# Optimization experiments

Measured on AMD Instinct MI355X. Metric: run time of the kernel, lower is better.

Reference implementation:

```python
import jax, jax.numpy as jnp
import numpy as np

N = 100000  # nodes
E = 3200000  # edges
NEG_SLOPE = 0.2  # GATConv default


def _gat_conv(x, src, dst, edge_attr, W, a_src, a_dst, W_e, a_e, bias):
    """PyG GATConv, heads=1, concat=True, add_self_loops=True (fill_value='mean')."""
    n = x.shape[0]
    loop = jnp.arange(n)
    s = jnp.concatenate([src, loop])
    d = jnp.concatenate([dst, loop])
    mean_ea = edge_attr.mean(axis=0)
    ea = jnp.concatenate([edge_attr, jnp.broadcast_to(mean_ea, (n, edge_attr.shape[1]))], axis=0)
    h = x @ W                          # [N, C]
    al_src = h @ a_src                 # [N]
    al_dst = h @ a_dst                 # [N]
    he = ea @ W_e                      # [E+N, C]
    alpha = al_src[s] + al_dst[d] + he @ a_e   # [E+N]
    alpha = jax.nn.leaky_relu(alpha, NEG_SLOPE)
    amax = jax.ops.segment_max(alpha, d, num_segments=n)
    ex = jnp.exp(alpha - amax[d])
    denom = jax.ops.segment_sum(ex, d, num_segments=n)
    coef = ex / (denom[d] + 1e-16)     # per-destination softmax (PyG softmax)
    out = jax.ops.segment_sum(h[s] * coef[:, None], d, num_segments=n)
    return out + bias


def _edge_mlp(z, w0, b0, w1, b1, w2, b2, w3, b3):
    z = jax.nn.relu(z @ w0 + b0)
    z = jax.nn.relu(z @ w1 + b1)
    z = jax.nn.relu(z @ w2 + b2)
    return z @ w3 + b3


def setup_inputs() -> dict:
    key = jax.random.key(0)
    ks = jax.random.split(key, 24)
    g = lambda i, sh, s=0.1: jax.random.normal(ks[i], sh, dtype=jnp.float32) * s
    return {
        "x": g(0, (N, 4), 1.0),
        "edge_attr": g(1, (E, 3), 1.0),
        "W1": g(2, (4, 16), 0.5), "as1": g(3, (16,)), "ad1": g(4, (16,)),
        "We1": g(5, (3, 16), 0.5), "ae1": g(6, (16,)), "b1": g(7, (16,)),
        "mw0": g(8, (35, 16), 0.17), "mb0": g(9, (16,)),
        "mw1": g(10, (16, 16), 0.25), "mb1": g(11, (16,)),
        "mw2": g(12, (16, 8), 0.25), "mb2": g(13, (8,)),
        "mw3": g(14, (8, 4), 0.35), "mb3": g(15, (4,)),
        "W2": g(16, (16, 2), 0.25), "as2": g(17, (2,)), "ad2": g(18, (2,)),
        "We2": g(19, (4, 2), 0.5), "ae2": g(20, (2,)), "b2": g(21, (2,)),
        "edge_index": jax.random.randint(ks[22], (2, E), 0, N),
    }


def reference(x, edge_attr, W1, as1, ad1, We1, ae1, b1,
              mw0, mb0, mw1, mb1, mw2, mb2, mw3, mb3,
              W2, as2, ad2, We2, ae2, b2, edge_index):
    src, dst = edge_index[0], edge_index[1]
    h = _gat_conv(x, src, dst, edge_attr, W1, as1, ad1, We1, ae1, b1)      # [N, 16]
    z = jnp.concatenate([h[src], edge_attr, h[dst]], axis=1)               # [E, 35]
    e = _edge_mlp(z, mw0, mb0, mw1, mb1, mw2, mb2, mw3, mb3)               # [E, 4]
    out = _gat_conv(h, src, dst, e, W2, as2, ad2, We2, ae2, b2)            # [N, 2]
    return jax.nn.log_softmax(out, axis=1), jax.nn.log_softmax(e, axis=1)
```

## Files before the change

### kernel.cpp

```cpp
#include <hip/hip_runtime.h>
#include <hip/hip_bf16.h>
#include <stdint.h>

typedef __hip_bfloat16 bf16;
typedef unsigned long long ull;
#define NT 256
#define EPT 4

__device__ __forceinline__ float b2f(bf16 v){ return __bfloat162float(v); }
__device__ __forceinline__ bf16 f2b(float v){ return __float2bfloat16(v); }
__device__ __forceinline__ float lrelu(float a){ return a>0.f ? a : 0.2f*a; }
__device__ __forceinline__ float sanf(float v){ return __builtin_isfinite(v) ? v : -12345.f; }
__device__ __forceinline__ float us2f(unsigned short u){ return __uint_as_float(((unsigned)u)<<16); }
__device__ __forceinline__ unsigned short f2bu(float v){ bf16 b=f2b(v); unsigned short u; __builtin_memcpy(&u,&b,2); return u; }

__device__ __forceinline__ float ld(const void* p, size_t i, int f32in){
  return f32in ? ((const float*)p)[i] : b2f(((const bf16*)p)[i]);
}

__device__ __forceinline__ float waveReduceSum(float v){
#pragma unroll
  for(int o=32;o>0;o>>=1) v += __shfl_down(v,o,64);
  return v;
}

__device__ __forceinline__ unsigned clampi(int v, int n){
  unsigned u=(unsigned)v; return (u<(unsigned)n)?u:0u;
}

__device__ __forceinline__ void load_h1v(const bf16* h1, unsigned node, float* dst){
  const ull* p=(const ull*)(h1+(size_t)node*16);
#pragma unroll
  for(int q=0;q<4;q++){
    ull v=p[q];
    dst[q*4+0]=us2f((unsigned short)v);        dst[q*4+1]=us2f((unsigned short)(v>>16));
    dst[q*4+2]=us2f((unsigned short)(v>>32));  dst[q*4+3]=us2f((unsigned short)(v>>48));
  }
}
__device__ __forceinline__ void load_x4(const void* x, unsigned n, int f32in, float* o){
  if(f32in){ float4 v=((const float4*)x)[n]; o[0]=v.x;o[1]=v.y;o[2]=v.z;o[3]=v.w; }
  else{
    ull v=((const ull*)x)[n];
    o[0]=us2f((unsigned short)v);       o[1]=us2f((unsigned short)(v>>16));
    o[2]=us2f((unsigned short)(v>>32)); o[3]=us2f((unsigned short)(v>>48));
  }
}

__global__ __launch_bounds__(64) void k_probe(const unsigned short* __restrict__ xraw,
                                              int nscan, float* __restrict__ stats){
  int t=threadIdx.x;
  int bad=0;
  for(int k=t*8;k<t*8+8;k++){
    if(k<nscan){
      unsigned short u=xraw[k];
      unsigned ex=(u>>7)&0xFF;
      bool plaus = (ex==0u) || (ex>=97u && ex<=157u);
      if(!plaus) bad++;
    }
  }
#pragma unroll
  for(int o=32;o>0;o>>=1) bad += __shfl_down(bad,o,64);
  if(t==0){
    for(int i=0;i<7;i++) stats[i]=0.f;
    ((int*)stats)[7] = (bad>=8) ? 1 : 0;
  }
}

__global__ __launch_bounds__(NT) void k_prep(const void* __restrict__ ea,
                                             const int* __restrict__ idx,
                                             int* __restrict__ rowc,
                                             float* __restrict__ stats, int E, int N){
  const int f32in=((const int*)stats)[7];
  __shared__ float lds[16];
  float s0=0.f,s1=0.f,s2=0.f;
  for(size_t e=(size_t)blockIdx.x*NT+threadIdx.x; e<(size_t)E; e+=(size_t)gridDim.x*NT){
    s0+=ld(ea,e*3+0,f32in); s1+=ld(ea,e*3+1,f32in); s2+=ld(ea,e*3+2,f32in);
    unsigned d=clampi(idx[(size_t)E+e],N);
    atomicAdd(&rowc[d],1);
  }
  int lane=threadIdx.x&63, wv=threadIdx.x>>6;
  s0=waveReduceSum(s0); s1=waveReduceSum(s1); s2=waveReduceSum(s2);
  if(lane==0){ lds[wv*4+0]=s0; lds[wv*4+1]=s1; lds[wv*4+2]=s2; }
  __syncthreads();
  if(threadIdx.x==0){
    float a0=0,a1=0,a2=0;
    for(int w=0;w<NT/64;w++){ a0+=lds[w*4]; a1+=lds[w*4+1]; a2+=lds[w*4+2]; }
    atomicAdd(&stats[0],a0); atomicAdd(&stats[1],a1); atomicAdd(&stats[2],a2);
  }
}

__global__ __launch_bounds__(NT) void k_node1(
    const void* __restrict__ x, const void* __restrict__ W1,
    const void* __restrict__ as1, const void* __restrict__ ad1,
    const float* __restrict__ stats,
    float* __restrict__ als, float* __restrict__ ald, int N){
  const int f32in=((const int*)stats)[7];
  __shared__ float sW1[64], sas[16], sad[16];
  if(threadIdx.x<64) sW1[threadIdx.x]=ld(W1,threadIdx.x,f32in);
  if(threadIdx.x<16){ sas[threadIdx.x]=ld(as1,threadIdx.x,f32in); sad[threadIdx.x]=ld(ad1,threadIdx.x,f32in); }
  __syncthreads();
  int i=blockIdx.x*NT+threadIdx.x;
  if(i>=N) return;
  float xv[4]; load_x4(x,(unsigned)i,f32in,xv);
  float a_s=0.f,a_d=0.f;
#pragma unroll
  for(int j=0;j<16;j++){
    float v=xv[0]*sW1[j]+xv[1]*sW1[16+j]+xv[2]*sW1[32+j]+xv[3]*sW1[48+j];
    a_s+=v*sas[j]; a_d+=v*sad[j];
  }
  als[i]=a_s; ald[i]=a_d;
}

__global__ __launch_bounds__(NT) void k_scan1(const int* __restrict__ rowc, int* __restrict__ bsum, int N){
  __shared__ int sm[NT];
  int i=blockIdx.x*NT+threadIdx.x;
  sm[threadIdx.x]=(i<N)?rowc[i]:0;
  __syncthreads();
  for(int o=NT/2;o>0;o>>=1){ if(threadIdx.x<o) sm[threadIdx.x]+=sm[threadIdx.x+o]; __syncthreads(); }
  if(threadIdx.x==0) bsum[blockIdx.x]=sm[0];
}
__global__ __launch_bounds__(1024) void k_scan2(int* __restrict__ bsum, int NB){
  __shared__ int sm[1024];
  int i=threadIdx.x;
  int v=(i<NB)?bsum[i]:0;
  sm[i]=v; __syncthreads();
  for(int o=1;o<1024;o<<=1){
    int t=(i>=o)?sm[i-o]:0; __syncthreads();
    sm[i]+=t; __syncthreads();
  }
  if(i<NB) bsum[i]=(i==0)?0:sm[i-1];
}
__global__ __launch_bounds__(NT) void k_scan3(int* __restrict__ rowc, const int* __restrict__ bsum, int N){
  __shared__ int sm[NT];
  int i=blockIdx.x*NT+threadIdx.x;
  int v=(i<N)?rowc[i]:0;
  sm[threadIdx.x]=v; __syncthreads();
  for(int o=1;o<NT;o<<=1){
    int t=(threadIdx.x>=o)?sm[threadIdx.x-o]:0; __syncthreads();
    sm[threadIdx.x]+=t; __syncthreads();
  }
  if(i<N) rowc[i]=bsum[blockIdx.x]+sm[threadIdx.x]-v;
}

__global__ __launch_bounds__(NT) void k_scatter(
    const int* __restrict__ idx, const void* __restrict__ ea,
    const void* __restrict__ We1, const void* __restrict__ ae1,
    const float* __restrict__ als, const float* __restrict__ stats,
    int* __restrict__ rowc, ull* __restrict__ csr, int E, int N){
  const int f32in=((const int*)stats)[7];
  __shared__ float sve[3];
  if(threadIdx.x<3){
    float v=0.f;
    for(int j=0;j<16;j++) v+=ld(We1,threadIdx.x*16+j,f32in)*ld(ae1,j,f32in);
    sve[threadIdx.x]=v;
  }
  __syncthreads();
  int e=blockIdx.x*NT+threadIdx.x;
  if(e>=E) return;
  unsigned s=clampi(idx[e],N), d=clampi(idx[(size_t)E+e],N);
  float ap = als[s] + ld(ea,(size_t)e*3+0,f32in)*sve[0]
                    + ld(ea,(size_t)e*3+1,f32in)*sve[1]
                    + ld(ea,(size_t)e*3+2,f32in)*sve[2];
  int pos=atomicAdd(&rowc[d],1);
  csr[pos] = (ull)s | ((ull)__float_as_uint(ap)<<32);
}

__global__ __launch_bounds__(NT) void k_gather1(
    const ull* __restrict__ csr, const int* __restrict__ rowe,
    const float* __restrict__ als, const float* __restrict__ ald,
    const void* __restrict__ x, const void* __restrict__ W1, const void* __restrict__ b1,
    const void* __restrict__ W2, const void* __restrict__ as2, const void* __restrict__ ad2,
    const void* __restrict__ We1, const void* __restrict__ ae1,
    const float* __restrict__ stats, float invE,
    bf16* __restrict__ h1, float* __restrict__ h2,
    float* __restrict__ als2, float* __restrict__ ald2, int N){
  const int f32in=((const int*)stats)[7];
  __shared__ float sW1[64], sb1[16], sW2[32], sas2[2], sad2[2], saea[1];
  if(threadIdx.x<64) sW1[threadIdx.x]=ld(W1,threadIdx.x,f32in);
  if(threadIdx.x<16) sb1[threadIdx.x]=ld(b1,threadIdx.x,f32in);
  if(threadIdx.x<32) sW2[threadIdx.x]=ld(W2,threadIdx.x,f32in);
  if(threadIdx.x<2){ sas2[threadIdx.x]=ld(as2,threadIdx.x,f32in); sad2[threadIdx.x]=ld(ad2,threadIdx.x,f32in); }
  if(threadIdx.x==0){
    float a=0.f;
    for(int k=0;k<3;k++){
      float v=0.f;
      for(int j=0;j<16;j++) v+=ld(We1,k*16+j,f32in)*ld(ae1,j,f32in);
      a+=stats[k]*v;
    }
    saea[0]=a*invE;
  }
  __syncthreads();
  int n=blockIdx.x*16+(threadIdx.x>>4);
  int c=threadIdx.x&15;
  if(n>=N) return;
  int end=rowe[n];
  int start=(n==0)?0:rowe[n-1];
  float aldn=ald[n], alsn=als[n];
  float aself=lrelu(alsn+aldn+saea[0]);
  float w0=sW1[c], w1=sW1[16+c], w2=sW1[32+c], w3=sW1[48+c];
  float m=aself;
  for(int k=start+c;k<end;k+=16){
    float ap=__uint_as_float((unsigned)(csr[k]>>32));
    m=fmaxf(m,lrelu(ap+aldn));
  }
#pragma unroll
  for(int o=1;o<16;o<<=1) m=fmaxf(m,__shfl_xor(m,o,64));
  float xv[4]; load_x4(x,(unsigned)n,f32in,xv);
  float hc_self=xv[0]*w0+xv[1]*w1+xv[2]*w2+xv[3]*w3;
  float exs=expf(fminf(aself-m,0.f));
  float den=exs, acc=exs*hc_self;
  for(int k=start;k<end;k++){
    ull v=csr[k];
    unsigned src=(unsigned)(v&0xffffffffu);
    float ap=__uint_as_float((unsigned)(v>>32));
    float ex=expf(fminf(lrelu(ap+aldn)-m,0.f));
    den+=ex;
    float xs[4]; load_x4(x,src,f32in,xs);
    float hc=xs[0]*w0+xs[1]*w1+xs[2]*w2+xs[3]*w3;
    acc+=ex*hc;
  }
  float inv=1.f/(den+1e-16f);
  float h1c=acc*inv+sb1[c];
  h1[(size_t)n*16+c]=f2b(h1c);
  float r0=h1c*sW2[c*2+0], r1=h1c*sW2[c*2+1];
#pragma unroll
  for(int o=1;o<16;o<<=1){ r0+=__shfl_xor(r0,o,64); r1+=__shfl_xor(r1,o,64); }
  if(c==0){
    h2[(size_t)n*2+0]=r0; h2[(size_t)n*2+1]=r1;
    als2[n]=r0*sas2[0]+r1*sas2[1];
    ald2[n]=r0*sad2[0]+r1*sad2[1];
  }
}

__global__ __launch_bounds__(NT) void k_wprep(
    const void* mw0,const void* mb0,const void* mw1,const void* mb1,
    const void* mw2,const void* mb2,const void* mw3,const void* mb3,
    const void* We2,const void* ae2,
    const float* __restrict__ stats, float* __restrict__ gw){
  const int f32in=((const int*)stats)[7];
  for(int t=threadIdx.x;t<560;t+=NT) gw[t]=ld(mw0,t,f32in);
  for(int t=threadIdx.x;t<256;t+=NT) gw[576+t]=ld(mw1,t,f32in);
  for(int t=threadIdx.x;t<128;t+=NT) gw[848+t]=ld(mw2,t,f32in);
  if(threadIdx.x<32) gw[984+threadIdx.x]=ld(mw3,threadIdx.x,f32in);
  if(threadIdx.x<16){ gw[560+threadIdx.x]=ld(mb0,threadIdx.x,f32in); gw[832+threadIdx.x]=ld(mb1,threadIdx.x,f32in); }
  if(threadIdx.x<8) gw[976+threadIdx.x]=ld(mb2,threadIdx.x,f32in);
  if(threadIdx.x<4){
    gw[1016+threadIdx.x]=ld(mb3,threadIdx.x,f32in);
    gw[1020+threadIdx.x]=ld(We2,threadIdx.x*2+0,f32in)*ld(ae2,0,f32in)
                        +ld(We2,threadIdx.x*2+1,f32in)*ld(ae2,1,f32in);
  }
}

__device__ __forceinline__ void mlp_eval_g4(const float z[EPT][35],
                                            const float* __restrict__ gw,
                                            float ev[EPT][4]){
  const float4* w4=(const float4*)gw;
  float t1[EPT][16];
  {
    const float4* b=(const float4*)(gw+560);
    float4 b0=b[0],b1=b[1],b2=b[2],b3=b[3];
#pragma unroll
    for(int u=0;u<EPT;u++){
      t1[u][0]=b0.x; t1[u][1]=b0.y; t1[u][2]=b0.z; t1[u][3]=b0.w;
      t1[u][4]=b1.x; t1[u][5]=b1.y; t1[u][6]=b1.z; t1[u][7]=b1.w;
      t1[u][8]=b2.x; t1[u][9]=b2.y; t1[u][10]=b2.z; t1[u][11]=b2.w;
      t1[u][12]=b3.x; t1[u][13]=b3.y; t1[u][14]=b3.z; t1[u][15]=b3.w;
    }
  }
#pragma unroll
  for(int i2=0;i2<35;i2++){
    float4 r0=w4[i2*4+0], r1=w4[i2*4+1], r2=w4[i2*4+2], r3=w4[i2*4+3];
#pragma unroll
    for(int u=0;u<EPT;u++){
      float a=z[u][i2];
      t1[u][0]+=a*r0.x; t1[u][1]+=a*r0.y; t1[u][2]+=a*r0.z; t1[u][3]+=a*r0.w;
      t1[u][4]+=a*r1.x; t1[u][5]+=a*r1.y; t1[u][6]+=a*r1.z; t1[u][7]+=a*r1.w;
      t1[u][8]+=a*r2.x; t1[u][9]+=a*r2.y; t1[u][10]+=a*r2.z; t1[u][11]+=a*r2.w;
      t1[u][12]+=a*r3.x; t1[u][13]+=a*r3.y; t1[u][14]+=a*r3.z; t1[u][15]+=a*r3.w;
    }
  }
#pragma unroll
  for(int u=0;u<EPT;u++)
#pragma unroll
    for(int j=0;j<16;j++) t1[u][j]=fmaxf(t1[u][j],0.f);

  const float4* w14=(const float4*)(gw+576);
  float t2[EPT][16];
  {
    const float4* b=(const float4*)(gw+832);
    float4 b0=b[0],b1=b[1],b2=b[2],b3=b[3];
#pragma unroll
    for(int u=0;u<EPT;u++){
      t2[u][0]=b0.x; t2[u][1]=b0.y; t2[u][2]=b0.z; t2[u][3]=b0.w;
      t2[u][4]=b1.x; t2[u][5]=b1.y; t2[u][6]=b1.z; t2[u][7]=b1.w;
      t2[u][8]=b2.x; t2[u][9]=b2.y; t2[u][10]=b2.z; t2[u][11]=b2.w;
      t2[u][12]=b3.x; t2[u][13]=b3.y; t2[u][14]=b3.z; t2[u][15]=b3.w;
    }
  }
#pragma unroll
  for(int i2=0;i2<16;i2++){
    float4 r0=w14[i2*4+0], r1=w14[i2*4+1], r2=w14[i2*4+2], r3=w14[i2*4+3];
#pragma unroll
    for(int u=0;u<EPT;u++){
      float a=t1[u][i2];
      t2[u][0]+=a*r0.x; t2[u][1]+=a*r0.y; t2[u][2]+=a*r0.z; t2[u][3]+=a*r0.w;
      t2[u][4]+=a*r1.x; t2[u][5]+=a*r1.y; t2[u][6]+=a*r1.z; t2[u][7]+=a*r1.w;
      t2[u][8]+=a*r2.x; t2[u][9]+=a*r2.y; t2[u][10]+=a*r2.z; t2[u][11]+=a*r2.w;
      t2[u][12]+=a*r3.x; t2[u][13]+=a*r3.y; t2[u][14]+=a*r3.z; t2[u][15]+=a*r3.w;
    }
  }
#pragma unroll
  for(int u=0;u<EPT;u++)
#pragma unroll
    for(int j=0;j<16;j++) t2[u][j]=fmaxf(t2[u][j],0.f);

  const float4* w24=(const float4*)(gw+848);
  float t3[EPT][8];
  {
    const float4* b=(const float4*)(gw+976);
    float4 b0=b[0],b1=b[1];
#pragma unroll
    for(int u=0;u<EPT;u++){
      t3[u][0]=b0.x; t3[u][1]=b0.y; t3[u][2]=b0.z; t3[u][3]=b0.w;
      t3[u][4]=b1.x; t3[u][5]=b1.y; t3[u][6]=b1.z; t3[u][7]=b1.w;
    }
  }
#pragma unroll
  for(int i2=0;i2<16;i2++){
    float4 r0=w24[i2*2+0], r1=w24[i2*2+1];
#pragma unroll
    for(int u=0;u<EPT;u++){
      float a=t2[u][i2];
      t3[u][0]+=a*r0.x; t3[u][1]+=a*r0.y; t3[u][2]+=a*r0.z; t3[u][3]+=a*r0.w;
      t3[u][4]+=a*r1.x; t3[u][5]+=a*r1.y; t3[u][6]+=a*r1.z; t3[u][7]+=a*r1.w;
    }
  }
#pragma unroll
  for(int u=0;u<EPT;u++)
#pragma unroll
    for(int j=0;j<8;j++) t3[u][j]=fmaxf(t3[u][j],0.f);

  const float4* w34=(const float4*)(gw+984);
  {
    const float4* b=(const float4*)(gw+1016);
    float4 b0=b[0];
#pragma unroll
    for(int u=0;u<EPT;u++){ ev[u][0]=b0.x; ev[u][1]=b0.y; ev[u][2]=b0.z; ev[u][3]=b0.w; }
  }
#pragma unroll
  for(int i2=0;i2<8;i2++){
    float4 r0=w34[i2];
#pragma unroll
    for(int u=0;u<EPT;u++){
      float a=t3[u][i2];
      ev[u][0]+=a*r0.x; ev[u][1]+=a*r0.y; ev[u][2]+=a*r0.z; ev[u][3]+=a*r0.w;
    }
  }
}

__device__ __forceinline__ void edge_epi(const float* ev, unsigned s, unsigned d, int e,
                                         const float* __restrict__ gw,
                                         const float* __restrict__ als2,
                                         const float* __restrict__ ald2,
                                         const float* __restrict__ h2,
                                         float* __restrict__ denom2, float* __restrict__ acc2,
                                         void* __restrict__ d_out, int f32in, int N){
  float m=fmaxf(fmaxf(ev[0],ev[1]),fmaxf(ev[2],ev[3]));
  float lse=m+logf(expf(ev[0]-m)+expf(ev[1]-m)+expf(ev[2]-m)+expf(ev[3]-m));
  if(f32in){
    float4 o; o.x=sanf(ev[0]-lse); o.y=sanf(ev[1]-lse); o.z=sanf(ev[2]-lse); o.w=sanf(ev[3]-lse);
    ((float4*)((float*)d_out+(size_t)2*N))[e]=o;
  }else{
    ull o = (ull)f2bu(sanf(ev[0]-lse))
          | ((ull)f2bu(sanf(ev[1]-lse))<<16)
          | ((ull)f2bu(sanf(ev[2]-lse))<<32)
          | ((ull)f2bu(sanf(ev[3]-lse))<<48);
    ((ull*)((bf16*)d_out+(size_t)2*N))[e]=o;
  }
  const float* s_ve2=gw+1020;
  float adot=ev[0]*s_ve2[0]+ev[1]*s_ve2[1]+ev[2]*s_ve2[2]+ev[3]*s_ve2[3];
  float a2=sanf(lrelu(als2[s]+ald2[d]+adot));
  float ex=expf(fminf(a2,80.f));
  float2 h2s=((const float2*)h2)[s];
  atomicAdd(&denom2[d],ex);
  atomicAdd(&acc2[(size_t)d*2+0],ex*h2s.x);
  atomicAdd(&acc2[(size_t)d*2+1],ex*h2s.y);
}

__global__ __launch_bounds__(NT,1) void k_edge2(
    const int* __restrict__ idx, const void* __restrict__ ea,
    const bf16* __restrict__ h1,
    const float* __restrict__ als2, const float* __restrict__ ald2,
    const float* __restrict__ gw,
    const float* __restrict__ h2,
    float* __restrict__ denom2, float* __restrict__ acc2,
    float* __restrict__ stats, void* __restrict__ d_out, int E, int N){
  const int f32in=((const int*)stats)[7];
  __shared__ float s_red[16];
  size_t base=(size_t)blockIdx.x*(NT*EPT)+threadIdx.x;
  int e[EPT]; bool v[EPT]; int es[EPT]; unsigned s[EPT], d[EPT];
#pragma unroll
  for(int u=0;u<EPT;u++){
    e[u]=(int)(base+(size_t)u*NT);
    v[u]=e[u]<E;
    es[u]=v[u]?e[u]:0;
    s[u]=clampi(idx[es[u]],N);
    d[u]=clampi(idx[(size_t)E+es[u]],N);
  }
  float z[EPT][35];
#pragma unroll
  for(int u=0;u<EPT;u++){
    load_h1v(h1,s[u],z[u]);
    load_h1v(h1,d[u],z[u]+19);
    z[u][16]=ld(ea,(size_t)es[u]*3+0,f32in);
    z[u][17]=ld(ea,(size_t)es[u]*3+1,f32in);
    z[u][18]=ld(ea,(size_t)es[u]*3+2,f32in);
  }
  float ev[EPT][4];
  mlp_eval_g4(z,gw,ev);
  float c0=0.f,c1=0.f,c2=0.f,c3=0.f;
#pragma unroll
  for(int u=0;u<EPT;u++){
    if(v[u]){
      edge_epi(ev[u],s[u],d[u],e[u],gw,als2,ald2,h2,denom2,acc2,d_out,f32in,N);
      c0+=ev[u][0]; c1+=ev[u][1]; c2+=ev[u][2]; c3+=ev[u][3];
    }
  }
  int lane=threadIdx.x&63, wv=threadIdx.x>>6;
  c0=waveReduceSum(c0); c1=waveReduceSum(c1); c2=waveReduceSum(c2); c3=waveReduceSum(c3);
  __syncthreads();
  if(lane==0){ s_red[wv*4]=c0; s_red[wv*4+1]=c1; s_red[wv*4+2]=c2; s_red[wv*4+3]=c3; }
  __syncthreads();
  if(threadIdx.x==0){
    float a0=0,a1=0,a2=0,a3=0;
    for(int w=0;w<NT/64;w++){ a0+=s_red[w*4]; a1+=s_red[w*4+1]; a2+=s_red[w*4+2]; a3+=s_red[w*4+3]; }
    atomicAdd(&stats[3],a0); atomicAdd(&stats[4],a1); atomicAdd(&stats[5],a2); atomicAdd(&stats[6],a3);
  }
}

__global__ __launch_bounds__(NT) void k_final(
    const float* __restrict__ stats, float invE,
    const float* __restrict__ als2, const float* __restrict__ ald2,
    const void* __restrict__ We2, const void* __restrict__ ae2,
    const float* __restrict__ h2,
    const float* __restrict__ denom2, const float* __restrict__ acc2,
    const void* __restrict__ bias2, void* __restrict__ d_out, int N){
  const int f32in=((const int*)stats)[7];
  __shared__ float s_ve2[4], s_b2[2];
  if(threadIdx.x<4)
    s_ve2[threadIdx.x]=ld(We2,threadIdx.x*2+0,f32in)*ld(ae2,0,f32in)
                      +ld(We2,threadIdx.x*2+1,f32in)*ld(ae2,1,f32in);
  if(threadIdx.x<2) s_b2[threadIdx.x]=ld(bias2,threadIdx.x,f32in);
  __syncthreads();
  int i=blockIdx.x*NT+threadIdx.x;
  if(i>=N) return;
  float adot=(stats[3]*s_ve2[0]+stats[4]*s_ve2[1]+stats[5]*s_ve2[2]+stats[6]*s_ve2[3])*invE;
  float self=lrelu(als2[i]+ald2[i]+adot);
  float ex=expf(fminf(self,80.f));
  float den=denom2[i]+ex;
  float inv=1.f/(den+1e-16f);
  float o0=(acc2[(size_t)i*2+0]+ex*h2[(size_t)i*2+0])*inv+s_b2[0];
  float o1=(acc2[(size_t)i*2+1]+ex*h2[(size_t)i*2+1])*inv+s_b2[1];
  float m=fmaxf(o0,o1);
  float lse=m+logf(expf(o0-m)+expf(o1-m));
  float r0=sanf(o0-lse), r1=sanf(o1-lse);
  if(f32in){
    float* o=(float*)d_out;
    o[(size_t)i*2+0]=r0; o[(size_t)i*2+1]=r1;
  }else{
    bf16* o=(bf16*)d_out;
    o[(size_t)i*2+0]=f2b(r0); o[(size_t)i*2+1]=f2b(r1);
  }
}

extern "C" void kernel_launch(void* const* d_in, const int* in_sizes, int n_in,
                              void* d_out, int out_size, void* d_ws, size_t ws_size,
                              hipStream_t stream){
  const void* x   =d_in[0];
  const void* ea  =d_in[1];
  const void* W1  =d_in[2];
  const void* as1 =d_in[3];
  const void* ad1 =d_in[4];
  const void* We1 =d_in[5];
  const void* ae1 =d_in[6];
  const void* b1  =d_in[7];
  const void* mw0 =d_in[8];
  const void* mb0 =d_in[9];
  const void* mw1 =d_in[10];
  const void* mb1 =d_in[11];
  const void* mw2 =d_in[12];
  const void* mb2 =d_in[13];
  const void* mw3 =d_in[14];
  const void* mb3 =d_in[15];
  const void* W2  =d_in[16];
  const void* as2 =d_in[17];
  const void* ad2 =d_in[18];
  const void* We2 =d_in[19];
  const void* ae2 =d_in[20];
  const void* bias2=d_in[21];
  const int*  idx =(const int*)d_in[22];

  int N=in_sizes[0]/4;
  int E=in_sizes[1]/3;
  float invE=1.f/(float)E;

  float*    F     =(float*)d_ws;
  float*    stats =F;
  float*    als   =F+8;
  float*    ald   =als+N;
  float*    ald2  =ald+N;
  int*      rowc  =(int*)(ald2+N);
  bf16*     h1    =(bf16*)(rowc+N);
  float*    h2    =(float*)(h1+(size_t)16*N);
  float*    acc2  =h2+(size_t)2*N;
  float*    den2  =ald;
  float*    gw    =(float*)((((uintptr_t)rowc)+15)&~(uintptr_t)15);

  ull* csr =(ull*)((char*)d_out+(size_t)4*N);
  int* bsum=(int*)((char*)d_out+(size_t)4*N);

  int NBn=(N+NT-1)/NT, nbE=(E+NT-1)/NT;
  int nbE4=(E+NT*EPT-1)/(NT*EPT);
  int nscan=in_sizes[0]*2; if(nscan>512) nscan=512;

  hipMemsetAsync(rowc,0,(size_t)N*sizeof(int),stream);
  k_probe  <<<1,64,0,stream>>>((const unsigned short*)x,nscan,stats);
  k_prep   <<<1024,NT,0,stream>>>(ea,idx,rowc,stats,E,N);
  k_node1  <<<NBn,NT,0,stream>>>(x,W1,as1,ad1,stats,als,ald,N);
  k_scan1  <<<NBn,NT,0,stream>>>(rowc,bsum,N);
  k_scan2  <<<1,1024,0,stream>>>(bsum,NBn);
  k_scan3  <<<NBn,NT,0,stream>>>(rowc,bsum,N);
  k_scatter<<<nbE,NT,0,stream>>>(idx,ea,We1,ae1,als,stats,rowc,csr,E,N);
  k_gather1<<<(N+15)/16,NT,0,stream>>>(csr,rowc,als,ald,x,W1,b1,W2,as2,ad2,We1,ae1,
                                       stats,invE,h1,h2,als,ald2,N);
  k_wprep  <<<1,NT,0,stream>>>(mw0,mb0,mw1,mb1,mw2,mb2,mw3,mb3,We2,ae2,stats,gw);
  hipMemsetAsync(den2,0,(size_t)N*sizeof(float),stream);
  hipMemsetAsync(acc2,0,(size_t)2*N*sizeof(float),stream);
  k_edge2  <<<nbE4,NT,0,stream>>>(idx,ea,h1,als,ald2,gw,h2,den2,acc2,stats,d_out,E,N);
  k_final  <<<NBn,NT,0,stream>>>(stats,invE,als,ald2,We2,ae2,h2,den2,acc2,bias2,d_out,N);
}
```

Before: 1.159 ms.

## Precompute per-node first MLP layer projections to cut per-edge FLOPs

Splits the first edge-MLP layer algebraically: the h[src] and h[dst] parts of the 35x16 product are computed once per node in a new kernel (k_upre) and stored as fp32 16-wide vectors. The edge kernel then gathers these two vectors, adds the 3-feature edge_attr term and the bias, and runs the remaining layers. This replaces 32 of the 35 input rows of per-edge multiply-adds with node-level work. In exchange each edge gathers 128 bytes of fp32 instead of 64 bytes of bf16 h1, and the edge kernel now uses launch_bounds(NT,2). The old path is kept as a fallback when the workspace is too small.

After: 1.134 ms. -2.2%, faster.

```diff
diff --git a/kernel.cpp b/kernel.cpp
--- a/kernel.cpp
+++ b/kernel.cpp
@@ -251,11 +251,127 @@
   }
 }
 
-__device__ __forceinline__ void mlp_eval_g4(const float z[EPT][35],
-                                            const float* __restrict__ gw,
-                                            float ev[EPT][4]){
+__global__ __launch_bounds__(NT) void k_upre(
+    const bf16* __restrict__ h1, const float* __restrict__ gw,
+    float* __restrict__ us, float* __restrict__ ud, int N){
+  int n=blockIdx.x*NT+threadIdx.x;
+  if(n>=N) return;
+  float h[16]; load_h1v(h1,(unsigned)n,h);
   const float4* w4=(const float4*)gw;
-  float t1[EPT][16];
+  float4 a0,a1,a2,a3;
+  { const float4* b=(const float4*)(gw+560); a0=b[0]; a1=b[1]; a2=b[2]; a3=b[3]; }
+#pragma unroll
+  for(int i=0;i<16;i++){
+    float z=h[i];
+    float4 r0=w4[i*4+0],r1=w4[i*4+1],r2=w4[i*4+2],r3=w4[i*4+3];
+    a0.x+=z*r0.x; a0.y+=z*r0.y; a0.z+=z*r0.z; a0.w+=z*r0.w;
+    a1.x+=z*r1.x; a1.y+=z*r1.y; a1.z+=z*r1.z; a1.w+=z*r1.w;
+    a2.x+=z*r2.x; a2.y+=z*r2.y; a2.z+=z*r2.z; a2.w+=z*r2.w;
+    a3.x+=z*r3.x; a3.y+=z*r3.y; a3.z+=z*r3.z; a3.w+=z*r3.w;
+  }
+  float4* po=(float4*)(us+(size_t)n*16);
+  po[0]=a0; po[1]=a1; po[2]=a2; po[3]=a3;
+  float4 c0=make_float4(0,0,0,0), c1=c0, c2=c0, c3=c0;
+#pragma unroll
+  for(int i=0;i<16;i++){
+    float z=h[i];
+    int r=19+i;
+    float4 r0=w4[r*4+0],r1=w4[r*4+1],r2=w4[r*4+2],r3=w4[r*4+3];
+    c0.x+=z*r0.x; c0.y+=z*r0.y; c0.z+=z*r0.z; c0.w+=z*r0.w;
+    c1.x+=z*r1.x; c1.y+=z*r1.y; c1.z+=z*r1.z; c1.w+=z*r1.w;
+    c2.x+=z*r2.x; c2.y+=z*r2.y; c2.z+=z*r2.z; c2.w+=z*r2.w;
+    c3.x+=z*r3.x; c3.y+=z*r3.y; c3.z+=z*r3.z; c3.w+=z*r3.w;
+  }
+  float4* pd=(float4*)(ud+(size_t)n*16);
+  pd[0]=c0; pd[1]=c1; pd[2]=c2; pd[3]=c3;
+}
+
+__device__ __forceinline__ void mlp_tail4(float t1[EPT][16],
+                                          const float* __restrict__ gw,
+                                          float ev[EPT][4]){
+#pragma unroll
+  for(int u=0;u<EPT;u++)
+#pragma unroll
+    for(int j=0;j<16;j++) t1[u][j]=fmaxf(t1[u][j],0.f);
+
+  const float4* w14=(const float4*)(gw+576);
+  float t2[EPT][16];
+  {
+    const float4* b=(const float4*)(gw+832);
+    float4 b0=b[0],b1=b[1],b2=b[2],b3=b[3];
+#pragma unroll
+    for(int u=0;u<EPT;u++){
+      t2[u][0]=b0.x; t2[u][1]=b0.y; t2[u][2]=b0.z; t2[u][3]=b0.w;
+      t2[u][4]=b1.x; t2[u][5]=b1.y; t2[u][6]=b1.z; t2[u][7]=b1.w;
+      t2[u][8]=b2.x; t2[u][9]=b2.y; t2[u][10]=b2.z; t2[u][11]=b2.w;
+      t2[u][12]=b3.x; t2[u][13]=b3.y; t2[u][14]=b3.z; t2[u][15]=b3.w;
+    }
+  }
+#pragma unroll
+  for(int i2=0;i2<16;i2++){
+    float4 r0=w14[i2*4+0], r1=w14[i2*4+1], r2=w14[i2*4+2], r3=w14[i2*4+3];
+#pragma unroll
+    for(int u=0;u<EPT;u++){
+      float a=t1[u][i2];
+      t2[u][0]+=a*r0.x; t2[u][1]+=a*r0.y; t2[u][2]+=a*r0.z; t2[u][3]+=a*r0.w;
+      t2[u][4]+=a*r1.x; t2[u][5]+=a*r1.y; t2[u][6]+=a*r1.z; t2[u][7]+=a*r1.w;
+      t2[u][8]+=a*r2.x; t2[u][9]+=a*r2.y; t2[u][10]+=a*r2.z; t2[u][11]+=a*r2.w;
+      t2[u][12]+=a*r3.x; t2[u][13]+=a*r3.y; t2[u][14]+=a*r3.z; t2[u][15]+=a*r3.w;
+    }
+  }
+#pragma unroll
+  for(int u=0;u<EPT;u++)
+#pragma unroll
+    for(int j=0;j<16;j++) t2[u][j]=fmaxf(t2[u][j],0.f);
+
+  const float4* w24=(const float4*)(gw+848);
+  float t3[EPT][8];
+  {
+    const float4* b=(const float4*)(gw+976);
+    float4 b0=b[0],b1=b[1];
+#pragma unroll
+    for(int u=0;u<EPT;u++){
+      t3[u][0]=b0.x; t3[u][1]=b0.y; t3[u][2]=b0.z; t3[u][3]=b0.w;
+      t3[u][4]=b1.x; t3[u][5]=b1.y; t3[u][6]=b1.z; t3[u][7]=b1.w;
+    }
+  }
+#pragma unroll
+  for(int i2=0;i2<16;i2++){
+    float4 r0=w24[i2*2+0], r1=w24[i2*2+1];
+#pragma unroll
+    for(int u=0;u<EPT;u++){
+      float a=t2[u][i2];
+      t3[u][0]+=a*r0.x; t3[u][1]+=a*r0.y; t3[u][2]+=a*r0.z; t3[u][3]+=a*r0.w;
+      t3[u][4]+=a*r1.x; t3[u][5]+=a*r1.y; t3[u][6]+=a*r1.z; t3[u][7]+=a*r1.w;
+    }
+  }
+#pragma unroll
+  for(int u=0;u<EPT;u++)
+#pragma unroll
+    for(int j=0;j<8;j++) t3[u][j]=fmaxf(t3[u][j],0.f);
+
+  const float4* w34=(const float4*)(gw+984);
+  {
+    const float4* b=(const float4*)(gw+1016);
+    float4 b0=b[0];
+#pragma unroll
+    for(int u=0;u<EPT;u++){ ev[u][0]=b0.x; ev[u][1]=b0.y; ev[u][2]=b0.z; ev[u][3]=b0.w; }
+  }
+#pragma unroll
+  for(int i2=0;i2<8;i2++){
+    float4 r0=w34[i2];
+#pragma unroll
+    for(int u=0;u<EPT;u++){
+      float a=t3[u][i2];
+      ev[u][0]+=a*r0.x; ev[u][1]+=a*r0.y; ev[u][2]+=a*r0.z; ev[u][3]+=a*r0.w;
+    }
+  }
+}
+
+__device__ __forceinline__ void mlp_head_full4(const float z[EPT][35],
+                                               const float* __restrict__ gw,
+                                               float t1[EPT][16]){
+  const float4* w4=(const float4*)gw;
   {
     const float4* b=(const float4*)(gw+560);
     float4 b0=b[0],b1=b[1],b2=b[2],b3=b[3];
@@ -277,83 +393,6 @@
       t1[u][4]+=a*r1.x; t1[u][5]+=a*r1.y; t1[u][6]+=a*r1.z; t1[u][7]+=a*r1.w;
       t1[u][8]+=a*r2.x; t1[u][9]+=a*r2.y; t1[u][10]+=a*r2.z; t1[u][11]+=a*r2.w;
       t1[u][12]+=a*r3.x; t1[u][13]+=a*r3.y; t1[u][14]+=a*r3.z; t1[u][15]+=a*r3.w;
-    }
-  }
-#pragma unroll
-  for(int u=0;u<EPT;u++)
-#pragma unroll
-    for(int j=0;j<16;j++) t1[u][j]=fmaxf(t1[u][j],0.f);
-
-  const float4* w14=(const float4*)(gw+576);
-  float t2[EPT][16];
-  {
-    const float4* b=(const float4*)(gw+832);
-    float4 b0=b[0],b1=b[1],b2=b[2],b3=b[3];
-#pragma unroll
-    for(int u=0;u<EPT;u++){
-      t2[u][0]=b0.x; t2[u][1]=b0.y; t2[u][2]=b0.z; t2[u][3]=b0.w;
-      t2[u][4]=b1.x; t2[u][5]=b1.y; t2[u][6]=b1.z; t2[u][7]=b1.w;
-      t2[u][8]=b2.x; t2[u][9]=b2.y; t2[u][10]=b2.z; t2[u][11]=b2.w;
-      t2[u][12]=b3.x; t2[u][13]=b3.y; t2[u][14]=b3.z; t2[u][15]=b3.w;
-    }
-  }
-#pragma unroll
-  for(int i2=0;i2<16;i2++){
-    float4 r0=w14[i2*4+0], r1=w14[i2*4+1], r2=w14[i2*4+2], r3=w14[i2*4+3];
-#pragma unroll
-    for(int u=0;u<EPT;u++){
-      float a=t1[u][i2];
-      t2[u][0]+=a*r0.x; t2[u][1]+=a*r0.y; t2[u][2]+=a*r0.z; t2[u][3]+=a*r0.w;
-      t2[u][4]+=a*r1.x; t2[u][5]+=a*r1.y; t2[u][6]+=a*r1.z; t2[u][7]+=a*r1.w;
-      t2[u][8]+=a*r2.x; t2[u][9]+=a*r2.y; t2[u][10]+=a*r2.z; t2[u][11]+=a*r2.w;
-      t2[u][12]+=a*r3.x; t2[u][13]+=a*r3.y; t2[u][14]+=a*r3.z; t2[u][15]+=a*r3.w;
-    }
-  }
-#pragma unroll
-  for(int u=0;u<EPT;u++)
-#pragma unroll
-    for(int j=0;j<16;j++) t2[u][j]=fmaxf(t2[u][j],0.f);
-
-  const float4* w24=(const float4*)(gw+848);
-  float t3[EPT][8];
-  {
-    const float4* b=(const float4*)(gw+976);
-    float4 b0=b[0],b1=b[1];
-#pragma unroll
-    for(int u=0;u<EPT;u++){
-      t3[u][0]=b0.x; t3[u][1]=b0.y; t3[u][2]=b0.z; t3[u][3]=b0.w;
-      t3[u][4]=b1.x; t3[u][5]=b1.y; t3[u][6]=b1.z; t3[u][7]=b1.w;
-    }
-  }
-#pragma unroll
-  for(int i2=0;i2<16;i2++){
-    float4 r0=w24[i2*2+0], r1=w24[i2*2+1];
-#pragma unroll
-    for(int u=0;u<EPT;u++){
-      float a=t2[u][i2];
-      t3[u][0]+=a*r0.x; t3[u][1]+=a*r0.y; t3[u][2]+=a*r0.z; t3[u][3]+=a*r0.w;
-      t3[u][4]+=a*r1.x; t3[u][5]+=a*r1.y; t3[u][6]+=a*r1.z; t3[u][7]+=a*r1.w;
-    }
-  }
-#pragma unroll
-  for(int u=0;u<EPT;u++)
-#pragma unroll
-    for(int j=0;j<8;j++) t3[u][j]=fmaxf(t3[u][j],0.f);
-
-  const float4* w34=(const float4*)(gw+984);
-  {
-    const float4* b=(const float4*)(gw+1016);
-    float4 b0=b[0];
-#pragma unroll
-    for(int u=0;u<EPT;u++){ ev[u][0]=b0.x; ev[u][1]=b0.y; ev[u][2]=b0.z; ev[u][3]=b0.w; }
-  }
-#pragma unroll
-  for(int i2=0;i2<8;i2++){
-    float4 r0=w34[i2];
-#pragma unroll
-    for(int u=0;u<EPT;u++){
-      float a=t3[u][i2];
-      ev[u][0]+=a*r0.x; ev[u][1]+=a*r0.y; ev[u][2]+=a*r0.z; ev[u][3]+=a*r0.w;
     }
   }
 }
@@ -387,6 +426,94 @@
   atomicAdd(&acc2[(size_t)d*2+1],ex*h2s.y);
 }
 
+__device__ __forceinline__ void stats_red(float c0,float c1,float c2,float c3,
+                                          float* s_red, float* stats){
+  int lane=threadIdx.x&63, wv=threadIdx.x>>6;
+  c0=waveReduceSum(c0); c1=waveReduceSum(c1); c2=waveReduceSum(c2); c3=waveReduceSum(c3);
+  __syncthreads();
+  if(lane==0){ s_red[wv*4]=c0; s_red[wv*4+1]=c1; s_red[wv*4+2]=c2; s_red[wv*4+3]=c3; }
+  __syncthreads();
+  if(threadIdx.x==0){
+    float a0=0,a1=0,a2=0,a3=0;
+    for(int w=0;w<NT/64;w++){ a0+=s_red[w*4]; a1+=s_red[w*4+1]; a2+=s_red[w*4+2]; a3+=s_red[w*4+3]; }
+    atomicAdd(&stats[3],a0); atomicAdd(&stats[4],a1); atomicAdd(&stats[5],a2); atomicAdd(&stats[6],a3);
+  }
+}
+
+__global__ __launch_bounds__(NT,2) void k_edge2s(
+    const int* __restrict__ idx, const void* __restrict__ ea,
+    const float* __restrict__ us, const float* __restrict__ ud,
+    const float* __restrict__ als2, const float* __restrict__ ald2,
+    const float* __restrict__ gw,
+    const float* __restrict__ h2,
+    float* __restrict__ denom2, float* __restrict__ acc2,
+    float* __restrict__ stats, void* __restrict__ d_out, int E, int N){
+  const int f32in=((const int*)stats)[7];
+  __shared__ float s_red[16];
+  size_t base=(size_t)blockIdx.x*(NT*EPT)+threadIdx.x;
+  int e[EPT]; bool v[EPT]; int es[EPT]; unsigned s[EPT], d[EPT];
+#pragma unroll
+  for(int u=0;u<EPT;u++){
+    e[u]=(int)(base+(size_t)u*NT);
+    v[u]=e[u]<E;
+    es[u]=v[u]?e[u]:0;
+    s[u]=clampi(idx[es[u]],N);
+    d[u]=clampi(idx[(size_t)E+es[u]],N);
+  }
+  float t1[EPT][16];
+#pragma unroll
+  for(int u=0;u<EPT;u++){
+    const float4* p=(const float4*)(us+(size_t)s[u]*16);
+    float4 a0=p[0],a1=p[1],a2=p[2],a3=p[3];
+    t1[u][0]=a0.x; t1[u][1]=a0.y; t1[u][2]=a0.z; t1[u][3]=a0.w;
+    t1[u][4]=a1.x; t1[u][5]=a1.y; t1[u][6]=a1.z; t1[u][7]=a1.w;
+    t1[u][8]=a2.x; t1[u][9]=a2.y; t1[u][10]=a2.z; t1[u][11]=a2.w;
+    t1[u][12]=a3.x; t1[u][13]=a3.y; t1[u][14]=a3.z; t1[u][15]=a3.w;
+  }
+  {
+    const float4* w16=(const float4*)(gw+256);
+    const float4* w17=(const float4*)(gw+272);
+    const float4* w18=(const float4*)(gw+288);
+    float4 q0[3]={w16[0],w17[0],w18[0]}, q1[3]={w16[1],w17[1],w18[1]},
+           q2[3]={w16[2],w17[2],w18[2]}, q3[3]={w16[3],w17[3],w18[3]};
+#pragma unroll
+    for(int u=0;u<EPT;u++){
+      float e3[3];
+      e3[0]=ld(ea,(size_t)es[u]*3+0,f32in);
+      e3[1]=ld(ea,(size_t)es[u]*3+1,f32in);
+      e3[2]=ld(ea,(size_t)es[u]*3+2,f32in);
+#pragma unroll
+      for(int k=0;k<3;k++){
+        float a=e3[k];
+        t1[u][0]+=a*q0[k].x; t1[u][1]+=a*q0[k].y; t1[u][2]+=a*q0[k].z; t1[u][3]+=a*q0[k].w;
+        t1[u][4]+=a*q1[k].x; t1[u][5]+=a*q1[k].y; t1[u][6]+=a*q1[k].z; t1[u][7]+=a*q1[k].w;
+        t1[u][8]+=a*q2[k].x; t1[u][9]+=a*q2[k].y; t1[u][10]+=a*q2[k].z; t1[u][11]+=a*q2[k].w;
+        t1[u][12]+=a*q3[k].x; t1[u][13]+=a*q3[k].y; t1[u][14]+=a*q3[k].z; t1[u][15]+=a*q3[k].w;
+      }
+    }
+  }
+#pragma unroll
+  for(int u=0;u<EPT;u++){
+    const float4* p=(const float4*)(ud+(size_t)d[u]*16);
+    float4 a0=p[0],a1=p[1],a2=p[2],a3=p[3];
+    t1[u][0]+=a0.x; t1[u][1]+=a0.y; t1[u][2]+=a0.z; t1[u][3]+=a0.w;
+    t1[u][4]+=a1.x; t1[u][5]+=a1.y; t1[u][6]+=a1.z; t1[u][7]+=a1.w;
+    t1[u][8]+=a2.x; t1[u][9]+=a2.y; t1[u][10]+=a2.z; t1[u][11]+=a2.w;
+    t1[u][12]+=a3.x; t1[u][13]+=a3.y; t1[u][14]+=a3.z; t1[u][15]+=a3.w;
+  }
+  float ev[EPT][4];
+  mlp_tail4(t1,gw,ev);
+  float c0=0.f,c1=0.f,c2=0.f,c3=0.f;
+#pragma unroll
+  for(int u=0;u<EPT;u++){
+    if(v[u]){
+      edge_epi(ev[u],s[u],d[u],e[u],gw,als2,ald2,h2,denom2,acc2,d_out,f32in,N);
+      c0+=ev[u][0]; c1+=ev[u][1]; c2+=ev[u][2]; c3+=ev[u][3];
+    }
+  }
+  stats_red(c0,c1,c2,c3,s_red,stats);
+}
+
 __global__ __launch_bounds__(NT,1) void k_edge2(
     const int* __restrict__ idx, const void* __restrict__ ea,
     const bf16* __restrict__ h1,
@@ -416,8 +543,10 @@
     z[u][17]=ld(ea,(size_t)es[u]*3+1,f32in);
     z[u][18]=ld(ea,(size_t)es[u]*3+2,f32in);
   }
+  float t1[EPT][16];
+  mlp_head_full4(z,gw,t1);
   float ev[EPT][4];
-  mlp_eval_g4(z,gw,ev);
+  mlp_tail4(t1,gw,ev);
   float c0=0.f,c1=0.f,c2=0.f,c3=0.f;
 #pragma unroll
   for(int u=0;u<EPT;u++){
@@ -426,16 +555,7 @@
       c0+=ev[u][0]; c1+=ev[u][1]; c2+=ev[u][2]; c3+=ev[u][3];
     }
   }
-  int lane=threadIdx.x&63, wv=threadIdx.x>>6;
-  c0=waveReduceSum(c0); c1=waveReduceSum(c1); c2=waveReduceSum(c2); c3=waveReduceSum(c3);
-  __syncthreads();
-  if(lane==0){ s_red[wv*4]=c0; s_red[wv*4+1]=c1; s_red[wv*4+2]=c2; s_red[wv*4+3]=c3; }
-  __syncthreads();
-  if(threadIdx.x==0){
-    float a0=0,a1=0,a2=0,a3=0;
-    for(int w=0;w<NT/64;w++){ a0+=s_red[w*4]; a1+=s_red[w*4+1]; a2+=s_red[w*4+2]; a3+=s_red[w*4+3]; }
-    atomicAdd(&stats[3],a0); atomicAdd(&stats[4],a1); atomicAdd(&stats[5],a2); atomicAdd(&stats[6],a3);
-  }
+  stats_red(c0,c1,c2,c3,s_red,stats);
 }
 
 __global__ __launch_bounds__(NT) void k_final(
@@ -515,6 +635,10 @@
   float*    acc2  =h2+(size_t)2*N;
   float*    den2  =ald;
   float*    gw    =(float*)((((uintptr_t)rowc)+15)&~(uintptr_t)15);
+  float*    u_s   =(float*)((((uintptr_t)(acc2+(size_t)2*N))+15)&~(uintptr_t)15);
+  float*    u_d   =u_s+(size_t)16*N;
+  size_t    need  =(size_t)((char*)(u_d+(size_t)16*N)-(char*)d_ws);
+  int use_split   =(ws_size>=need)?1:0;
 
   ull* csr =(ull*)((char*)d_out+(size_t)4*N);
   int* bsum=(int*)((char*)d_out+(size_t)4*N);
@@ -536,6 +660,11 @@
   k_wprep  <<<1,NT,0,stream>>>(mw0,mb0,mw1,mb1,mw2,mb2,mw3,mb3,We2,ae2,stats,gw);
   hipMemsetAsync(den2,0,(size_t)N*sizeof(float),stream);
   hipMemsetAsync(acc2,0,(size_t)2*N*sizeof(float),stream);
-  k_edge2  <<<nbE4,NT,0,stream>>>(idx,ea,h1,als,ald2,gw,h2,den2,acc2,stats,d_out,E,N);
+  if(use_split){
+    k_upre   <<<NBn,NT,0,stream>>>(h1,gw,u_s,u_d,N);
+    k_edge2s <<<nbE4,NT,0,stream>>>(idx,ea,u_s,u_d,als,ald2,gw,h2,den2,acc2,stats,d_out,E,N);
+  }else{
+    k_edge2  <<<nbE4,NT,0,stream>>>(idx,ea,h1,als,ald2,gw,h2,den2,acc2,stats,d_out,E,N);
+  }
   k_final  <<<NBn,NT,0,stream>>>(stats,invE,als,ald2,We2,ae2,h2,den2,acc2,bias2,d_out,N);
 }
```
